# Performance work log

Hardware: AMD Instinct MI355X
Metric: run time of the kernel (lower is better)

## Reference

```python
import jax, jax.numpy as jnp
import numpy as np

D_IN, D_BIAS, H, DH = 256, 128, 8, 32

def _layernorm(x, w, b, eps=1e-5):
    mu = jnp.mean(x, axis=-1, keepdims=True)
    var = jnp.var(x, axis=-1, keepdims=True)
    return (x - mu) * jax.lax.rsqrt(var + eps) * w + b

def setup_inputs() -> dict:
    key = jax.random.key(0)
    ks = jax.random.split(key, 8)
    B, L = 1, 768
    x = jax.random.normal(ks[0], (B, L, D_IN), dtype=jnp.float32)
    bias = jax.random.normal(ks[1], (B, L, L, D_BIAS), dtype=jnp.float32)
    s_in = 1.0 / np.sqrt(D_IN)
    s_b = 1.0 / np.sqrt(D_BIAS)
    return {
        "x": x,
        "bias": bias,
        "ln_in_w": jnp.ones((D_IN,), jnp.float32),
        "ln_in_b": jnp.zeros((D_IN,), jnp.float32),
        "ln_b_w": jnp.ones((D_BIAS,), jnp.float32),
        "ln_b_b": jnp.zeros((D_BIAS,), jnp.float32),
        "Wq": jax.random.normal(ks[2], (D_IN, H * DH), jnp.float32) * s_in,
        "Wk": jax.random.normal(ks[3], (D_IN, H * DH), jnp.float32) * s_in,
        "Wv": jax.random.normal(ks[4], (D_IN, H * DH), jnp.float32) * s_in,
        "Wb": jax.random.normal(ks[5], (D_BIAS, H), jnp.float32) * s_b,
        "Wg": jax.random.normal(ks[6], (D_IN, H * DH), jnp.float32) * 0.02,
        "bg": jnp.ones((H * DH,), jnp.float32),
        "Wo": jax.random.normal(ks[7], (H * DH, D_IN), jnp.float32) * 0.02,
        "bo": jnp.zeros((D_IN,), jnp.float32),
    }

def reference(x, bias, ln_in_w, ln_in_b, ln_b_w, ln_b_b, Wq, Wk, Wv, Wb, Wg, bg, Wo, bo):
    B, L, _ = x.shape
    scaling = 1.0 / np.sqrt(DH)
    xn = _layernorm(x, ln_in_w, ln_in_b)            # (B,L,D_IN)
    bn = _layernorm(bias, ln_b_w, ln_b_b)           # (B,L,L,D_BIAS)
    q = (xn @ Wq).reshape(B, L, H, DH)
    k = (xn @ Wk).reshape(B, L, H, DH) * scaling
    v = (xn @ Wv).reshape(B, L, H, DH)
    b = bn @ Wb                                     # (B,L,L,H)
    gate = jax.nn.sigmoid(xn @ Wg + bg)             # (B,L,H*DH)
    attn = jnp.einsum('bqhd,bkhd->bqkh', q, k) + b  # (B,q,k,h)
    attn = jax.nn.softmax(attn, axis=2)             # softmax over key dim
    out = jnp.einsum('bqkh,bkhd->bqhd', attn, v).reshape(B, L, H * DH)
    out = gate * out
    return out @ Wo + bo
```

## Files before the change

kernel.cpp:

```cpp
#include <hip/hip_runtime.h>

#define LQ 768
#define DIN 256
#define DB 128
#define NH 8
#define DH 32

#define OFF_QB 0
#define OFF_KT (LQ*DIN)
#define OFF_VB (2*LQ*DIN)
#define OFF_GB (3*LQ*DIN)
#define OFF_W2 (4*LQ*DIN)
#define OFF_SC (OFF_W2 + DB*NH)
#define OFF_LG (OFF_SC + 16)

__device__ __forceinline__ void gload_lds16(const void* g, void* l) {
    __builtin_amdgcn_global_load_lds(
        (__attribute__((address_space(1))) const void*)g,
        (__attribute__((address_space(3))) void*)l,
        16, 0, 0);
}

__global__ __launch_bounds__(128) void setup_kernel(
    const float* __restrict__ lbw, const float* __restrict__ lbb,
    const float* __restrict__ Wb, float* __restrict__ W2, float* __restrict__ SC)
{
    const int d = threadIdx.x;
    const int lane = d & 63, wv = d >> 6;
    float w = lbw[d], b = lbb[d];
    float pS[NH], pC[NH];
    #pragma unroll
    for (int h = 0; h < NH; h++) {
        float wb = Wb[d*NH + h];
        float w2 = w * wb;
        W2[d*NH + h] = w2;
        pS[h] = w2;
        pC[h] = b * wb;
    }
    #pragma unroll
    for (int m = 1; m <= 32; m <<= 1) {
        #pragma unroll
        for (int h = 0; h < NH; h++) { pS[h] += __shfl_xor(pS[h], m); pC[h] += __shfl_xor(pC[h], m); }
    }
    __shared__ float red[2][16];
    if (lane == 0) {
        #pragma unroll
        for (int h = 0; h < NH; h++) { red[wv][h] = pS[h]; red[wv][NH+h] = pC[h]; }
    }
    __syncthreads();
    if (d < 16) SC[d] = red[0][d] + red[1][d];
}

__global__ __launch_bounds__(256) void proj_kernel(
    const float* __restrict__ x, const float* __restrict__ lnw, const float* __restrict__ lnb,
    const float* __restrict__ Wq, const float* __restrict__ Wk, const float* __restrict__ Wv,
    const float* __restrict__ Wg, const float* __restrict__ bg,
    float* __restrict__ qb, float* __restrict__ kT, float* __restrict__ vb, float* __restrict__ gb)
{
    const int tid = threadIdx.x;
    const int lane = tid & 63, rr = tid >> 6;
    const int row = blockIdx.x * 4 + rr;
    __shared__ float xn[4][DIN];

    float4 xv = ((const float4*)x)[row * (DIN/4) + lane];
    float s  = xv.x + xv.y + xv.z + xv.w;
    float ss = xv.x*xv.x + xv.y*xv.y + xv.z*xv.z + xv.w*xv.w;
    #pragma unroll
    for (int m = 1; m <= 32; m <<= 1) { s += __shfl_xor(s, m); ss += __shfl_xor(ss, m); }
    float mu  = s * (1.0f/DIN);
    float inv = rsqrtf(ss * (1.0f/DIN) - mu*mu + 1e-5f);
    float4 wv4 = ((const float4*)lnw)[lane];
    float4 bv4 = ((const float4*)lnb)[lane];
    float4 r4;
    r4.x = (xv.x - mu)*inv*wv4.x + bv4.x;
    r4.y = (xv.y - mu)*inv*wv4.y + bv4.y;
    r4.z = (xv.z - mu)*inv*wv4.z + bv4.z;
    r4.w = (xv.w - mu)*inv*wv4.w + bv4.w;
    *((float4*)&xn[rr][lane*4]) = r4;
    __syncthreads();

    const int col = tid;
    float aq[4] = {0,0,0,0}, ak[4] = {0,0,0,0}, av[4] = {0,0,0,0}, ag[4] = {0,0,0,0};
    for (int i4 = 0; i4 < DIN/4; i4++) {
        float4 x0 = *((const float4*)&xn[0][i4*4]);
        float4 x1 = *((const float4*)&xn[1][i4*4]);
        float4 x2 = *((const float4*)&xn[2][i4*4]);
        float4 x3 = *((const float4*)&xn[3][i4*4]);
        const float* p0 = (const float*)&x0;
        const float* p1 = (const float*)&x1;
        const float* p2 = (const float*)&x2;
        const float* p3 = (const float*)&x3;
        #pragma unroll
        for (int e = 0; e < 4; e++) {
            const int i = i4*4 + e;
            float wq = Wq[i*DIN + col], wk = Wk[i*DIN + col];
            float wvv = Wv[i*DIN + col], wg = Wg[i*DIN + col];
            aq[0] = fmaf(p0[e], wq, aq[0]); aq[1] = fmaf(p1[e], wq, aq[1]);
            aq[2] = fmaf(p2[e], wq, aq[2]); aq[3] = fmaf(p3[e], wq, aq[3]);
            ak[0] = fmaf(p0[e], wk, ak[0]); ak[1] = fmaf(p1[e], wk, ak[1]);
            ak[2] = fmaf(p2[e], wk, ak[2]); ak[3] = fmaf(p3[e], wk, ak[3]);
            av[0] = fmaf(p0[e], wvv, av[0]); av[1] = fmaf(p1[e], wvv, av[1]);
            av[2] = fmaf(p2[e], wvv, av[2]); av[3] = fmaf(p3[e], wvv, av[3]);
            ag[0] = fmaf(p0[e], wg, ag[0]); ag[1] = fmaf(p1[e], wg, ag[1]);
            ag[2] = fmaf(p2[e], wg, ag[2]); ag[3] = fmaf(p3[e], wg, ag[3]);
        }
    }
    const float kscale = 0.17677669529663687f;
    float bgv = bg[col];
    #pragma unroll
    for (int r = 0; r < 4; r++) {
        const int orow = blockIdx.x*4 + r;
        qb[orow*DIN + col] = aq[r];
        vb[orow*DIN + col] = av[r];
        gb[orow*DIN + col] = 1.0f/(1.0f + __expf(-(ag[r] + bgv)));
    }
    *((float4*)&kT[col*LQ + blockIdx.x*4]) =
        make_float4(ak[0]*kscale, ak[1]*kscale, ak[2]*kscale, ak[3]*kscale);
}

__global__ __launch_bounds__(128) void bias_kernel(
    const float* __restrict__ bias, const float* __restrict__ W2g,
    const float* __restrict__ SCg, float* __restrict__ logits)
{
    __shared__ float tile[2][2][2048];
    __shared__ float w2p[4*264];

    const int tid  = threadIdx.x;
    const int q    = blockIdx.y;
    const int w    = tid >> 6;
    const int lane = tid & 63;
    const int key  = lane & 15;
    const int q4   = lane >> 4;
    const int kwave = blockIdx.x * 128 + w * 64;

    for (int j = tid; j < 4*264; j += 128) {
        int g = j >> 8;
        g = j / 264;
        int rem = j - g*264;
        w2p[j] = (rem < 256) ? W2g[g*256 + rem] : 0.0f;
    }
    __syncthreads();

    float Sh[NH], Ch[NH];
    #pragma unroll
    for (int h = 0; h < NH; h++) { Sh[h] = SCg[h]; Ch[h] = SCg[NH + h]; }

    const char* gbase = (const char*)(bias + ((size_t)q*LQ + kwave)*DB);
    char* const lbase0 = (char*)&tile[0][w][0];
    char* const lbase1 = (char*)&tile[1][w][0];

    #define STAGE(t, lb)                                                     \
        {                                                                    \
            const char* gs = gbase + (size_t)(t)*8192;                       \
            _Pragma("unroll")                                                \
            for (int c = 0; c < 8; c++) {                                    \
                int L  = c*1024 + lane*16;                                   \
                int sw = L ^ (((L >> 9) & 15) << 4);                         \
                gload_lds16(gs + sw, (lb) + c*1024);                         \
            }                                                                \
        }

    STAGE(0, lbase0);
    asm volatile("" ::: "memory");
    STAGE(1, lbase1);

    const int rbase0 = ((key << 9) | (q4 << 7)) ^ (key << 4);

    #pragma unroll
    for (int t = 0; t < 4; t++) {
        if (t == 0)      asm volatile("s_waitcnt vmcnt(8)"  ::: "memory");
        else if (t < 3)  asm volatile("s_waitcnt vmcnt(10)" ::: "memory");
        else             asm volatile("s_waitcnt vmcnt(0)"  ::: "memory");

        const char* tw = (t & 1) ? lbase1 : lbase0;
        float s = 0.f, ss = 0.f;
        float acc[NH] = {0,0,0,0,0,0,0,0};
        #pragma unroll
        for (int j = 0; j < 8; j++) {
            float4 v = *(const float4*)(tw + (rbase0 ^ (j << 4)));
            const float* wp = &w2p[q4*264 + j*32];
            #pragma unroll
            for (int e = 0; e < 4; e++) {
                float xv = (&v.x)[e];
                s += xv; ss = fmaf(xv, xv, ss);
                float4 w0 = *(const float4*)(wp + e*8);
                float4 w1 = *(const float4*)(wp + e*8 + 4);
                acc[0] = fmaf(xv, w0.x, acc[0]); acc[1] = fmaf(xv, w0.y, acc[1]);
                acc[2] = fmaf(xv, w0.z, acc[2]); acc[3] = fmaf(xv, w0.w, acc[3]);
                acc[4] = fmaf(xv, w1.x, acc[4]); acc[5] = fmaf(xv, w1.y, acc[5]);
                acc[6] = fmaf(xv, w1.z, acc[6]); acc[7] = fmaf(xv, w1.w, acc[7]);
            }
        }
        #pragma unroll
        for (int m = 16; m <= 32; m <<= 1) {
            s += __shfl_xor(s, m); ss += __shfl_xor(ss, m);
            #pragma unroll
            for (int h = 0; h < NH; h++) acc[h] += __shfl_xor(acc[h], m);
        }
        if (q4 == 0) {
            float mu  = s * (1.0f/DB);
            float inv = rsqrtf(ss * (1.0f/DB) - mu*mu + 1e-5f);
            float lo[NH];
            #pragma unroll
            for (int h = 0; h < NH; h++)
                lo[h] = fmaf(inv, acc[h] - mu*Sh[h], Ch[h]);
            float4* dst = (float4*)(logits + ((size_t)q*LQ + kwave + t*16 + key)*NH);
            dst[0] = make_float4(lo[0], lo[1], lo[2], lo[3]);
            dst[1] = make_float4(lo[4], lo[5], lo[6], lo[7]);
        }
        asm volatile("" ::: "memory");
        if (t + 2 < 4) {
            char* nb = (t & 1) ? lbase1 : lbase0;
            STAGE(t + 2, nb);
        }
    }
    #undef STAGE
}

__global__ __launch_bounds__(256) void attn_kernel(
    const float* __restrict__ logits, const float* __restrict__ qbuf,
    const float* __restrict__ kT, const float* __restrict__ vbuf,
    const float* __restrict__ gb, const float* __restrict__ Wo,
    const float* __restrict__ bo, float* __restrict__ out)
{
    const int tid = threadIdx.x;
    const int q0 = blockIdx.x * 2;
    __shared__ float pT[2][NH][776];
    __shared__ float ao[2][DIN];
    __shared__ float isum[2][NH];

    #pragma unroll
    for (int r = 0; r < 2; r++) {
        const float4* rp = (const float4*)(logits + (size_t)(q0 + r)*LQ*NH);
        #pragma unroll
        for (int ii = 0; ii < 6; ii++) {
            int jj = ii*256 + tid;
            float4 t = rp[jj];
            int k = jj >> 1, h0 = (jj & 1) << 2;
            pT[r][h0+0][k] = t.x; pT[r][h0+1][k] = t.y;
            pT[r][h0+2][k] = t.z; pT[r][h0+3][k] = t.w;
        }
    }
    __syncthreads();

    if (tid < 192) {
        const float* q0p = qbuf + (size_t)q0*DIN;
        const float* q1p = q0p + DIN;
        #pragma unroll
        for (int h = 0; h < NH; h++) {
            float a00=0,a01=0,a02=0,a03=0, a10=0,a11=0,a12=0,a13=0;
            #pragma unroll
            for (int dd = 0; dd < DH; dd++) {
                const int d = h*DH + dd;
                float4 kv = *(const float4*)(kT + (size_t)d*LQ + tid*4);
                float qa = q0p[d], qc = q1p[d];
                a00 = fmaf(qa, kv.x, a00); a01 = fmaf(qa, kv.y, a01);
                a02 = fmaf(qa, kv.z, a02); a03 = fmaf(qa, kv.w, a03);
                a10 = fmaf(qc, kv.x, a10); a11 = fmaf(qc, kv.y, a11);
                a12 = fmaf(qc, kv.z, a12); a13 = fmaf(qc, kv.w, a13);
            }
            float4 p0 = *(float4*)&pT[0][h][tid*4];
            p0.x += a00; p0.y += a01; p0.z += a02; p0.w += a03;
            *(float4*)&pT[0][h][tid*4] = p0;
            float4 p1 = *(float4*)&pT[1][h][tid*4];
            p1.x += a10; p1.y += a11; p1.z += a12; p1.w += a13;
            *(float4*)&pT[1][h][tid*4] = p1;
        }
    }
    __syncthreads();

    {
        const int r = tid >> 7, h = (tid >> 4) & 7, l = tid & 15;
        float4* row = (float4*)&pT[r][h][0];
        float m = -1e30f;
        for (int i = l; i < 192; i += 16) {
            float4 v = row[i];
            m = fmaxf(m, fmaxf(fmaxf(v.x, v.y), fmaxf(v.z, v.w)));
        }
        #pragma unroll
        for (int mm = 1; mm <= 8; mm <<= 1) m = fmaxf(m, __shfl_xor(m, mm));
        float sum = 0.f;
        for (int i = l; i < 192; i += 16) {
            float4 v = row[i];
            v.x = __expf(v.x - m); v.y = __expf(v.y - m);
            v.z = __expf(v.z - m); v.w = __expf(v.w - m);
            sum += v.x + v.y + v.z + v.w;
            row[i] = v;
        }
        #pragma unroll
        for (int mm = 1; mm <= 8; mm <<= 1) sum += __shfl_xor(sum, mm);
        if (l == 0) isum[r][h] = 1.0f / sum;
    }
    __syncthreads();

    {
        const int h = tid >> 5, d = tid & 31;
        const float* vp = vbuf + h*DH + d;
        const float4* p0r = (const float4*)&pT[0][h][0];
        const float4* p1r = (const float4*)&pT[1][h][0];
        float a0 = 0.f, a1 = 0.f;
        for (int k4 = 0; k4 < 192; k4++) {
            float4 p0 = p0r[k4], p1 = p1r[k4];
            float v0 = vp[(size_t)(k4*4+0)*DIN];
            float v1 = vp[(size_t)(k4*4+1)*DIN];
            float v2 = vp[(size_t)(k4*4+2)*DIN];
            float v3 = vp[(size_t)(k4*4+3)*DIN];
            a0 = fmaf(p0.x, v0, a0); a0 = fmaf(p0.y, v1, a0);
            a0 = fmaf(p0.z, v2, a0); a0 = fmaf(p0.w, v3, a0);
            a1 = fmaf(p1.x, v0, a1); a1 = fmaf(p1.y, v1, a1);
            a1 = fmaf(p1.z, v2, a1); a1 = fmaf(p1.w, v3, a1);
        }
        ao[0][tid] = a0 * isum[0][h] * gb[(q0+0)*DIN + tid];
        ao[1][tid] = a1 * isum[1][h] * gb[(q0+1)*DIN + tid];
    }
    __syncthreads();

    {
        const int col = tid;
        float o0 = bo[col], o1 = o0;
        for (int i = 0; i < DIN; i++) {
            float wv = Wo[i*DIN + col];
            o0 = fmaf(ao[0][i], wv, o0);
            o1 = fmaf(ao[1][i], wv, o1);
        }
        out[(q0+0)*DIN + col] = o0;
        out[(q0+1)*DIN + col] = o1;
    }
}

extern "C" void kernel_launch(void* const* d_in, const int* in_sizes, int n_in,
                              void* d_out, int out_size, void* d_ws, size_t ws_size,
                              hipStream_t stream) {
    const float* x    = (const float*)d_in[0];
    const float* bias = (const float*)d_in[1];
    const float* lnw  = (const float*)d_in[2];
    const float* lnb  = (const float*)d_in[3];
    const float* lbw  = (const float*)d_in[4];
    const float* lbb  = (const float*)d_in[5];
    const float* Wq   = (const float*)d_in[6];
    const float* Wk   = (const float*)d_in[7];
    const float* Wv   = (const float*)d_in[8];
    const float* Wb   = (const float*)d_in[9];
    const float* Wg   = (const float*)d_in[10];
    const float* bg   = (const float*)d_in[11];
    const float* Wo   = (const float*)d_in[12];
    const float* bo   = (const float*)d_in[13];

    float* ws = (float*)d_ws;
    float* qb = ws + OFF_QB;
    float* kT = ws + OFF_KT;
    float* vb = ws + OFF_VB;
    float* gb = ws + OFF_GB;
    float* W2 = ws + OFF_W2;
    float* SC = ws + OFF_SC;
    float* lg = ws + OFF_LG;

    setup_kernel<<<1, 128, 0, stream>>>(lbw, lbb, Wb, W2, SC);
    proj_kernel<<<LQ/4, 256, 0, stream>>>(x, lnw, lnb, Wq, Wk, Wv, Wg, bg, qb, kT, vb, gb);
    bias_kernel<<<dim3(6, LQ), 128, 0, stream>>>(bias, W2, SC, lg);
    attn_kernel<<<LQ/2, 256, 0, stream>>>(lg, qb, kT, vb, gb, Wo, bo, (float*)d_out);
}
```

Measured before the change: 158.5 us.

## Restructure bias layernorm kernel as persistent waves with register prefetch

The bias kernel becomes a fixed grid of 512 blocks. Each wave handles 9 consecutive 64-key tiles. Instead of async global-to-LDS DMA with swizzling, the next tile is prefetched into 32 float4 registers, then written to a padded per-wave LDS tile (row stride 129) that gives conflict-free one-row-per-lane reads. Each lane computes a full 128-element row reduction with W2 read directly from global (uniform scalar loads), so the cross-lane shuffle reductions go away. In exchange it uses about 128 extra VGPRs and a large LDS footprint (about 66KB per block), which limits occupancy to about 2 blocks per CU and gives less memory-level parallelism for this bandwidth-bound stream.

```diff
diff --git a/kernel.cpp b/kernel.cpp
--- a/kernel.cpp
+++ b/kernel.cpp
@@ -13,13 +13,6 @@
 #define OFF_W2 (4*LQ*DIN)
 #define OFF_SC (OFF_W2 + DB*NH)
 #define OFF_LG (OFF_SC + 16)
-
-__device__ __forceinline__ void gload_lds16(const void* g, void* l) {
-    __builtin_amdgcn_global_load_lds(
-        (__attribute__((address_space(1))) const void*)g,
-        (__attribute__((address_space(3))) void*)l,
-        16, 0, 0);
-}
 
 __global__ __launch_bounds__(128) void setup_kernel(
     const float* __restrict__ lbw, const float* __restrict__ lbb,
@@ -122,99 +115,86 @@
     const float* __restrict__ bias, const float* __restrict__ W2g,
     const float* __restrict__ SCg, float* __restrict__ logits)
 {
-    __shared__ float tile[2][2][2048];
-    __shared__ float w2p[4*264];
-
+    __shared__ float tile[2][64 * 129];
     const int tid  = threadIdx.x;
-    const int q    = blockIdx.y;
     const int w    = tid >> 6;
     const int lane = tid & 63;
-    const int key  = lane & 15;
-    const int q4   = lane >> 4;
-    const int kwave = blockIdx.x * 128 + w * 64;
-
-    for (int j = tid; j < 4*264; j += 128) {
-        int g = j >> 8;
-        g = j / 264;
-        int rem = j - g*264;
-        w2p[j] = (rem < 256) ? W2g[g*256 + rem] : 0.0f;
-    }
-    __syncthreads();
+    const int wid  = blockIdx.x * 2 + w;
+
+    float* tw = &tile[w][0];
+    const int wbase = (lane >> 5) * 129 + (lane & 31) * 4;
+    const int rbase = lane * 129;
 
     float Sh[NH], Ch[NH];
     #pragma unroll
     for (int h = 0; h < NH; h++) { Sh[h] = SCg[h]; Ch[h] = SCg[NH + h]; }
 
-    const char* gbase = (const char*)(bias + ((size_t)q*LQ + kwave)*DB);
-    char* const lbase0 = (char*)&tile[0][w][0];
-    char* const lbase1 = (char*)&tile[1][w][0];
-
-    #define STAGE(t, lb)                                                     \
-        {                                                                    \
-            const char* gs = gbase + (size_t)(t)*8192;                       \
-            _Pragma("unroll")                                                \
-            for (int c = 0; c < 8; c++) {                                    \
-                int L  = c*1024 + lane*16;                                   \
-                int sw = L ^ (((L >> 9) & 15) << 4);                         \
-                gload_lds16(gs + sw, (lb) + c*1024);                         \
-            }                                                                \
-        }
-
-    STAGE(0, lbase0);
-    asm volatile("" ::: "memory");
-    STAGE(1, lbase1);
-
-    const int rbase0 = ((key << 9) | (q4 << 7)) ^ (key << 4);
-
-    #pragma unroll
-    for (int t = 0; t < 4; t++) {
-        if (t == 0)      asm volatile("s_waitcnt vmcnt(8)"  ::: "memory");
-        else if (t < 3)  asm volatile("s_waitcnt vmcnt(10)" ::: "memory");
-        else             asm volatile("s_waitcnt vmcnt(0)"  ::: "memory");
-
-        const char* tw = (t & 1) ? lbase1 : lbase0;
+    float4 v[32];
+
+    const int tau0 = wid * 9;
+
+    {
+        const int q  = tau0 / 12;
+        const int kb = (tau0 % 12) * 64;
+        const float4* gs = (const float4*)(bias + ((size_t)q * LQ + kb) * DB);
+        #pragma unroll
+        for (int c = 0; c < 32; c++) v[c] = gs[c * 64 + lane];
+        #pragma unroll
+        for (int c = 0; c < 32; c++) {
+            tw[wbase + c*258 + 0] = v[c].x;
+            tw[wbase + c*258 + 1] = v[c].y;
+            tw[wbase + c*258 + 2] = v[c].z;
+            tw[wbase + c*258 + 3] = v[c].w;
+        }
+    }
+
+    for (int t = 0; t < 9; t++) {
+        const int tau = tau0 + t;
+
+        if (t + 1 < 9) {
+            const int qn  = (tau + 1) / 12;
+            const int kbn = ((tau + 1) % 12) * 64;
+            const float4* gs = (const float4*)(bias + ((size_t)qn * LQ + kbn) * DB);
+            #pragma unroll
+            for (int c = 0; c < 32; c++) v[c] = gs[c * 64 + lane];
+        }
+        asm volatile("" ::: "memory");
+
         float s = 0.f, ss = 0.f;
         float acc[NH] = {0,0,0,0,0,0,0,0};
-        #pragma unroll
-        for (int j = 0; j < 8; j++) {
-            float4 v = *(const float4*)(tw + (rbase0 ^ (j << 4)));
-            const float* wp = &w2p[q4*264 + j*32];
-            #pragma unroll
-            for (int e = 0; e < 4; e++) {
-                float xv = (&v.x)[e];
-                s += xv; ss = fmaf(xv, xv, ss);
-                float4 w0 = *(const float4*)(wp + e*8);
-                float4 w1 = *(const float4*)(wp + e*8 + 4);
-                acc[0] = fmaf(xv, w0.x, acc[0]); acc[1] = fmaf(xv, w0.y, acc[1]);
-                acc[2] = fmaf(xv, w0.z, acc[2]); acc[3] = fmaf(xv, w0.w, acc[3]);
-                acc[4] = fmaf(xv, w1.x, acc[4]); acc[5] = fmaf(xv, w1.y, acc[5]);
-                acc[6] = fmaf(xv, w1.z, acc[6]); acc[7] = fmaf(xv, w1.w, acc[7]);
-            }
-        }
-        #pragma unroll
-        for (int m = 16; m <= 32; m <<= 1) {
-            s += __shfl_xor(s, m); ss += __shfl_xor(ss, m);
-            #pragma unroll
-            for (int h = 0; h < NH; h++) acc[h] += __shfl_xor(acc[h], m);
-        }
-        if (q4 == 0) {
+        #pragma unroll 4
+        for (int d = 0; d < DB; d++) {
+            float xv = tw[rbase + d];
+            const float* wr = W2g + d * NH;
+            s += xv; ss = fmaf(xv, xv, ss);
+            #pragma unroll
+            for (int h = 0; h < NH; h++) acc[h] = fmaf(xv, wr[h], acc[h]);
+        }
+
+        {
+            const int q  = tau / 12;
+            const int kb = (tau % 12) * 64;
             float mu  = s * (1.0f/DB);
             float inv = rsqrtf(ss * (1.0f/DB) - mu*mu + 1e-5f);
             float lo[NH];
             #pragma unroll
             for (int h = 0; h < NH; h++)
-                lo[h] = fmaf(inv, acc[h] - mu*Sh[h], Ch[h]);
-            float4* dst = (float4*)(logits + ((size_t)q*LQ + kwave + t*16 + key)*NH);
+                lo[h] = fmaf(inv, fmaf(-mu, Sh[h], acc[h]), Ch[h]);
+            float4* dst = (float4*)(logits + ((size_t)q*LQ + kb + lane)*NH);
             dst[0] = make_float4(lo[0], lo[1], lo[2], lo[3]);
             dst[1] = make_float4(lo[4], lo[5], lo[6], lo[7]);
         }
-        asm volatile("" ::: "memory");
-        if (t + 2 < 4) {
-            char* nb = (t & 1) ? lbase1 : lbase0;
-            STAGE(t + 2, nb);
-        }
-    }
-    #undef STAGE
+
+        if (t + 1 < 9) {
+            #pragma unroll
+            for (int c = 0; c < 32; c++) {
+                tw[wbase + c*258 + 0] = v[c].x;
+                tw[wbase + c*258 + 1] = v[c].y;
+                tw[wbase + c*258 + 2] = v[c].z;
+                tw[wbase + c*258 + 3] = v[c].w;
+            }
+        }
+    }
 }
 
 __global__ __launch_bounds__(256) void attn_kernel(
@@ -357,6 +337,6 @@
 
     setup_kernel<<<1, 128, 0, stream>>>(lbw, lbb, Wb, W2, SC);
     proj_kernel<<<LQ/4, 256, 0, stream>>>(x, lnw, lnb, Wq, Wk, Wv, Wg, bg, qb, kT, vb, gb);
-    bias_kernel<<<dim3(6, LQ), 128, 0, stream>>>(bias, W2, SC, lg);
+    bias_kernel<<<512, 128, 0, stream>>>(bias, W2, SC, lg);
     attn_kernel<<<LQ/2, 256, 0, stream>>>(lg, qb, kT, vb, gb, Wo, bo, (float*)d_out);
 }
```

Result: slower. 164.0 us (+3.5%).
